# Kernel optimization log

Hardware: AMD Instinct MI355X
Metric: run time of the kernel (lower is better)

Reference implementation:

```python
import jax, jax.numpy as jnp
import numpy as np

N = 100_000      # nodes
F_IN = 256       # input features
HID = 256        # hidden dim
C = 40           # classes
E = 1_600_000    # edges
BN_EPS = 1e-5


def setup_inputs() -> dict:
    key = jax.random.key(0)
    ks = jax.random.split(key, 8)
    x = jax.random.normal(ks[0], (N, F_IN), dtype=jnp.float32)
    edge_index = jax.random.randint(ks[1], (2, E), 0, N)
    W1 = jax.random.normal(ks[2], (F_IN, HID), dtype=jnp.float32) / np.sqrt(F_IN)
    b1 = jnp.zeros((HID,), jnp.float32)
    gamma = jnp.ones((HID,), jnp.float32)
    beta = jnp.zeros((HID,), jnp.float32)
    W2 = jax.random.normal(ks[3], (HID, C), dtype=jnp.float32) / np.sqrt(HID)
    b2 = jnp.zeros((C,), jnp.float32)
    return {"x": x, "edge_index": edge_index, "W1": W1, "b1": b1,
            "gamma": gamma, "beta": beta, "W2": W2, "b2": b2}


def _gcn_propagate(h, src, dst, norm):
    # out[dst] += norm * h[src]   (symmetric-normalized aggregation, self-loops included)
    msg = norm[:, None] * h[src]                       # [E+N, D]
    return jax.ops.segment_sum(msg, dst, num_segments=N)


def reference(x, edge_index, W1, b1, gamma, beta, W2, b2):
    loops = jnp.arange(N, dtype=edge_index.dtype)
    src = jnp.concatenate([edge_index[0], loops])      # add self-loops (PyG GCNConv)
    dst = jnp.concatenate([edge_index[1], loops])
    deg = jax.ops.segment_sum(jnp.ones_like(dst, jnp.float32), dst, num_segments=N)
    dinv = jnp.where(deg > 0, jax.lax.rsqrt(deg), 0.0)
    norm = dinv[src] * dinv[dst]

    # Layer 1: GCNConv (linear without bias -> propagate -> + bias)
    h = _gcn_propagate(x @ W1, src, dst, norm) + b1    # [N, HID]
    # BatchNorm1d over nodes (training-style batch statistics, biased variance)
    mu = h.mean(axis=0)
    var = h.var(axis=0)
    h = (h - mu) * jax.lax.rsqrt(var + BN_EPS) * gamma + beta
    h = jax.nn.relu(h)                                 # dropout is identity in eval

    # Layer 2: GCNConv -> log_softmax
    out = _gcn_propagate(h @ W2, src, dst, norm) + b2  # [N, C]
    return jax.nn.log_softmax(out, axis=1)
```

## Files before the change

kernel.cpp:

```cpp
#include <hip/hip_runtime.h>
#include <math.h>

#define N_NODES 100000
#define F_IN    256
#define HID     256
#define C_OUT   40
#define N_EDGES 1600000
#define BN_EPS  1e-5f

#define CAP     64
#define NSHARD  8
#define CNT_BLOCKS  ((N_EDGES + 255) / 256)

typedef __attribute__((ext_vector_type(8))) short short8;
typedef __attribute__((ext_vector_type(8))) unsigned short ushort8v;
typedef __attribute__((ext_vector_type(4))) float f32x4;

static __device__ __forceinline__ unsigned short f2bf(float f) {
    unsigned int u = __float_as_uint(f);
    unsigned int r = u + 0x7FFFu + ((u >> 16) & 1u);
    return (unsigned short)(r >> 16);
}
static __device__ __forceinline__ float bf2f(unsigned short b) {
    return __uint_as_float(((unsigned int)b) << 16);
}

__global__ void count_castw(const int* __restrict__ dst, int* cnt8,
                            int* __restrict__ rank,
                            const float* __restrict__ W1, const float* __restrict__ W2,
                            unsigned short* __restrict__ w1t, unsigned short* __restrict__ w2t) {
    int b = blockIdx.x, t = threadIdx.x;
    if (b < CNT_BLOCKS) {
        int i = b * 256 + t;
        if (i < N_EDGES) {
            int s = b & (NSHARD - 1);
            rank[i] = atomicAdd(&cnt8[s * N_NODES + dst[i]], 1);
        }
    } else if (b < CNT_BLOCKS + 256) {
        int n = b - CNT_BLOCKS;
        w1t[(size_t)n * 256 + t] = f2bf(W1[(size_t)t * 256 + n]);
    } else {
        int n = b - CNT_BLOCKS - 256;
        w2t[(size_t)n * 256 + t] = (n < C_OUT) ? f2bf(W2[(size_t)t * C_OUT + n]) : (unsigned short)0;
    }
}

__global__ __launch_bounds__(256) void base_init(const int* __restrict__ cnt8,
                                                 int* __restrict__ base8,
                                                 int* __restrict__ cnttot,
                                                 float* __restrict__ dinv) {
    int d = blockIdx.x * 256 + threadIdx.x;
    if (d < N_NODES) {
        int run = 0;
#pragma unroll
        for (int s = 0; s < NSHARD; s++) {
            int c = cnt8[s * N_NODES + d];
            base8[s * N_NODES + d] = run;
            run += c;
        }
        cnttot[d] = run;
        dinv[d] = rsqrtf((float)(run + 1));
    }
}

__global__ __launch_bounds__(256) void scatter_sharded(const int* __restrict__ src,
                                                       const int* __restrict__ dst,
                                                       const int* __restrict__ rank,
                                                       const int* __restrict__ base8,
                                                       int* __restrict__ csr) {
    int e = blockIdx.x * 256 + threadIdx.x;
    if (e < N_EDGES) {
        int s = (e >> 8) & (NSHARD - 1);
        int d = dst[e];
        int pos = base8[s * N_NODES + d] + rank[e];
        if (pos < CAP) csr[(size_t)d * CAP + pos] = src[e];
    }
}

#define LDK 56
__global__ __launch_bounds__(256) void gemm1_mfma(const float* __restrict__ x,
                                                  const unsigned short* __restrict__ w1t,
                                                  const float* __restrict__ dinv,
                                                  unsigned short* __restrict__ hs, int M) {
    __shared__ unsigned short As[64][LDK];
    __shared__ unsigned short Bs[256][LDK];
    int tid = threadIdx.x;
    int wave = tid >> 6, lane = tid & 63;
    int m0 = blockIdx.x * 64;
    f32x4 acc[4][4] = {};

    int ar = tid >> 2, ac = (tid & 3) * 8;
    int brow = tid;
    int gr = m0 + ar;
    bool rowok = gr < M;
    const float* xrow = x + (size_t)gr * 256 + ac;
    const unsigned short* wrow = w1t + (size_t)brow * 256;

    float4 pa = make_float4(0.f,0.f,0.f,0.f), pb = pa;
    if (rowok) { pa = *(const float4*)(xrow); pb = *(const float4*)(xrow + 4); }
    ushort8v rb0 = *(const ushort8v*)(wrow);
    ushort8v rb1 = *(const ushort8v*)(wrow + 8);
    ushort8v rb2 = *(const ushort8v*)(wrow + 16);
    ushort8v rb3 = *(const ushort8v*)(wrow + 24);

    for (int k0 = 0; k0 < 256; k0 += 32) {
        {
            ushort8v u;
            u[0] = f2bf(pa.x); u[1] = f2bf(pa.y); u[2] = f2bf(pa.z); u[3] = f2bf(pa.w);
            u[4] = f2bf(pb.x); u[5] = f2bf(pb.y); u[6] = f2bf(pb.z); u[7] = f2bf(pb.w);
            if (!rowok) {
#pragma unroll
                for (int q = 0; q < 8; q++) u[q] = 0;
            }
            *(ushort8v*)&As[ar][ac] = u;
        }
        *(ushort8v*)&Bs[brow][0]  = rb0;
        *(ushort8v*)&Bs[brow][8]  = rb1;
        *(ushort8v*)&Bs[brow][16] = rb2;
        *(ushort8v*)&Bs[brow][24] = rb3;
        __syncthreads();
        if (k0 + 32 < 256) {
            if (rowok) {
                pa = *(const float4*)(xrow + k0 + 32);
                pb = *(const float4*)(xrow + k0 + 36);
            }
            const unsigned short* p = wrow + k0 + 32;
            rb0 = *(const ushort8v*)(p);
            rb1 = *(const ushort8v*)(p + 8);
            rb2 = *(const ushort8v*)(p + 16);
            rb3 = *(const ushort8v*)(p + 24);
        }
        int fr = lane & 15, fk = (lane >> 4) * 8;
        short8 a[4], b[4];
#pragma unroll
        for (int mt = 0; mt < 4; mt++) a[mt] = *(short8*)&As[mt * 16 + fr][fk];
#pragma unroll
        for (int nt = 0; nt < 4; nt++) b[nt] = *(short8*)&Bs[wave * 64 + nt * 16 + fr][fk];
#pragma unroll
        for (int mt = 0; mt < 4; mt++)
#pragma unroll
            for (int nt = 0; nt < 4; nt++)
                acc[mt][nt] = __builtin_amdgcn_mfma_f32_16x16x32_bf16(a[mt], b[nt], acc[mt][nt], 0, 0, 0);
        __syncthreads();
    }
    int fr = lane & 15, fg = lane >> 4;
#pragma unroll
    for (int mt = 0; mt < 4; mt++) {
#pragma unroll
        for (int r = 0; r < 4; r++) {
            int row = m0 + mt * 16 + fg * 4 + r;
            if (row < M) {
                float dv = dinv[row];
#pragma unroll
                for (int nt = 0; nt < 4; nt++) {
                    int col = wave * 64 + nt * 16 + fr;
                    hs[(size_t)row * 256 + col] = f2bf(acc[mt][nt][r] * dv);
                }
            }
        }
    }
}

__global__ __launch_bounds__(256) void agg256(const int* __restrict__ cnttot,
                                              const int* __restrict__ csr,
                                              const unsigned short* __restrict__ hs,
                                              const float* __restrict__ dinv,
                                              unsigned short* __restrict__ hagg) {
    int g = blockIdx.x * blockDim.x + threadIdx.x;
    int wid = g >> 6, lane = g & 63;
    if (wid >= N_NODES) return;
    int half = lane >> 5;
    int c8 = (lane & 31) * 8;
    int beg = wid * CAP;
    int end = beg + min(cnttot[wid], CAP);
    float acc[8] = {0.f, 0.f, 0.f, 0.f, 0.f, 0.f, 0.f, 0.f};
    int j = beg;
    if (j + 7 < end) {
        int sxA[4];
        ushort8v uA[4];
#pragma unroll
        for (int q = 0; q < 4; q++) sxA[q] = csr[j + 2 * q + half];
#pragma unroll
        for (int q = 0; q < 4; q++) uA[q] = *(const ushort8v*)(hs + (size_t)sxA[q] * 256 + c8);
        j += 8;
        while (j + 7 < end) {
            int sxB[4];
            ushort8v uB[4];
#pragma unroll
            for (int q = 0; q < 4; q++) sxB[q] = csr[j + 2 * q + half];
#pragma unroll
            for (int q = 0; q < 4; q++) uB[q] = *(const ushort8v*)(hs + (size_t)sxB[q] * 256 + c8);
#pragma unroll
            for (int q = 0; q < 4; q++)
#pragma unroll
                for (int e = 0; e < 8; e++) acc[e] += bf2f(uA[q][e]);
#pragma unroll
            for (int q = 0; q < 4; q++) uA[q] = uB[q];
            j += 8;
        }
#pragma unroll
        for (int q = 0; q < 4; q++)
#pragma unroll
            for (int e = 0; e < 8; e++) acc[e] += bf2f(uA[q][e]);
    }
    if (j + 3 < end) {
        int s0 = csr[j + half];
        int s1 = csr[j + 2 + half];
        ushort8v u0 = *(const ushort8v*)(hs + (size_t)s0 * 256 + c8);
        ushort8v u1 = *(const ushort8v*)(hs + (size_t)s1 * 256 + c8);
#pragma unroll
        for (int e = 0; e < 8; e++) acc[e] += bf2f(u0[e]) + bf2f(u1[e]);
        j += 4;
    }
    if (j + 1 < end) {
        int s = csr[j + half];
        ushort8v u = *(const ushort8v*)(hs + (size_t)s * 256 + c8);
#pragma unroll
        for (int e = 0; e < 8; e++) acc[e] += bf2f(u[e]);
        j += 2;
    }
    if (j < end && half == 0) {
        int s = csr[j];
        ushort8v u = *(const ushort8v*)(hs + (size_t)s * 256 + c8);
#pragma unroll
        for (int e = 0; e < 8; e++) acc[e] += bf2f(u[e]);
    }
#pragma unroll
    for (int e = 0; e < 8; e++) acc[e] += __shfl_xor(acc[e], 32);
    if (half == 0) {
        ushort8v us = *(const ushort8v*)(hs + (size_t)wid * 256 + c8);
        float dv = dinv[wid];
        ushort8v o;
#pragma unroll
        for (int e = 0; e < 8; e++) o[e] = f2bf((acc[e] + bf2f(us[e])) * dv);
        *(ushort8v*)(hagg + (size_t)wid * 256 + c8) = o;
    }
}

#define BNS_BLOCKS 1024
__global__ __launch_bounds__(256) void bn_stats_v(const unsigned short* __restrict__ h,
                                                  float* musum, float* sqsum) {
    int tid = threadIdx.x;
    int wave = tid >> 6, lane = tid & 63;
    int half = lane >> 5;
    int c8 = (lane & 31) * 8;
    int gw = blockIdx.x * 4 + wave;
    float s[8] = {0.f,0.f,0.f,0.f,0.f,0.f,0.f,0.f};
    float q2[8] = {0.f,0.f,0.f,0.f,0.f,0.f,0.f,0.f};
    for (int r = gw * 2 + half; r < N_NODES; r += BNS_BLOCKS * 4 * 2) {
        ushort8v u = *(const ushort8v*)(h + (size_t)r * 256 + c8);
#pragma unroll
        for (int e = 0; e < 8; e++) {
            float v = bf2f(u[e]);
            s[e] += v; q2[e] += v * v;
        }
    }
#pragma unroll
    for (int e = 0; e < 8; e++) {
        s[e]  += __shfl_xor(s[e], 32);
        q2[e] += __shfl_xor(q2[e], 32);
    }
    __shared__ float sS[4][256];
    __shared__ float sQ[4][256];
    if (half == 0) {
#pragma unroll
        for (int e = 0; e < 8; e++) { sS[wave][c8 + e] = s[e]; sQ[wave][c8 + e] = q2[e]; }
    }
    __syncthreads();
    float a = sS[0][tid] + sS[1][tid] + sS[2][tid] + sS[3][tid];
    float b = sQ[0][tid] + sQ[1][tid] + sQ[2][tid] + sQ[3][tid];
    atomicAdd(&musum[tid], a);
    atomicAdd(&sqsum[tid], b);
}

#define LDB2 264
__global__ __launch_bounds__(256) void gemm2_mfma(const unsigned short* __restrict__ hagg,
                                                  const unsigned short* __restrict__ w2t,
                                                  const float* __restrict__ musum,
                                                  const float* __restrict__ sqsum,
                                                  const float* __restrict__ gamma,
                                                  const float* __restrict__ beta,
                                                  const float* __restrict__ dinv,
                                                  unsigned short* __restrict__ g2b, int M) {
    __shared__ unsigned short w2s[48][LDB2];
    __shared__ unsigned short As[64][40];
    __shared__ float ss[256], sh[256];
    int tid = threadIdx.x;
    int wave = tid >> 6, lane = tid & 63;
    int m0 = blockIdx.x * 64;

    for (int i = tid; i < 48 * 32; i += 256) {
        int rrow = i >> 5, c8 = (i & 31) * 8;
        *(ushort8v*)&w2s[rrow][c8] = *(const ushort8v*)(w2t + (size_t)rrow * 256 + c8);
    }
    {
        const float invN = 1.0f / N_NODES;
        float m = musum[tid] * invN;
        float var = sqsum[tid] * invN - m * m;
        float s = gamma[tid] * rsqrtf(var + BN_EPS);
        ss[tid] = s;
        sh[tid] = beta[tid] - m * s;
    }

    f32x4 acc[3] = {};
    int arow = tid >> 2, ac0 = (tid & 3) * 8;
    int fr = lane & 15, fk = (lane >> 4) * 8;

    for (int k0 = 0; k0 < 256; k0 += 32) {
        __syncthreads();
        {
            int gr = m0 + arow;
            ushort8v u;
            if (gr < M) {
                u = *(const ushort8v*)(hagg + (size_t)gr * 256 + k0 + ac0);
#pragma unroll
                for (int q = 0; q < 8; q++) {
                    int col = k0 + ac0 + q;
                    float v = bf2f(u[q]);
                    v = fmaxf(v * ss[col] + sh[col], 0.0f);
                    u[q] = f2bf(v);
                }
            } else {
#pragma unroll
                for (int q = 0; q < 8; q++) u[q] = 0;
            }
            *(ushort8v*)&As[arow][ac0] = u;
        }
        __syncthreads();
        short8 a = *(short8*)&As[wave * 16 + fr][fk];
#pragma unroll
        for (int nt = 0; nt < 3; nt++) {
            short8 b = *(short8*)&w2s[nt * 16 + fr][k0 + fk];
            acc[nt] = __builtin_amdgcn_mfma_f32_16x16x32_bf16(a, b, acc[nt], 0, 0, 0);
        }
    }
    int fg = lane >> 4;
#pragma unroll
    for (int nt = 0; nt < 3; nt++) {
        int col = nt * 16 + fr;
        if (col < C_OUT) {
#pragma unroll
            for (int r = 0; r < 4; r++) {
                int row = m0 + wave * 16 + fg * 4 + r;
                if (row < M) g2b[(size_t)row * C_OUT + col] = f2bf(acc[nt][r] * dinv[row]);
            }
        }
    }
}

__global__ __launch_bounds__(256) void agg40_logsm(const int* __restrict__ cnttot,
                                                   const int* __restrict__ csr,
                                                   const unsigned short* __restrict__ g2b,
                                                   const float* __restrict__ dinv,
                                                   const float* __restrict__ b2,
                                                   float* __restrict__ out) {
    int gi = blockIdx.x * blockDim.x + threadIdx.x;
    int wid = gi >> 6, lane = gi & 63;
    if (wid >= N_NODES) return;
    int g = lane / 10;
    int k4 = lane - g * 10;
    bool gact = lane < 60;
    int beg = wid * CAP;
    int end = beg + min(cnttot[wid], CAP);
    float a4[4] = {0.f, 0.f, 0.f, 0.f};
    if (end > beg) {
        int jlim = end - 1;
        int j = beg;
        int s0 = csr[min(j + g, jlim)];
        ushort4 u0 = *(const ushort4*)(g2b + (size_t)s0 * C_OUT + k4 * 4);
        while (1) {
            int jn = j + 6;
            bool more = jn < end;
            int s1 = 0; ushort4 u1;
            if (more) {
                s1 = csr[min(jn + g, jlim)];
                u1 = *(const ushort4*)(g2b + (size_t)s1 * C_OUT + k4 * 4);
            }
            if (gact && j + g < end) {
                a4[0] += bf2f(u0.x); a4[1] += bf2f(u0.y);
                a4[2] += bf2f(u0.z); a4[3] += bf2f(u0.w);
            }
            if (!more) break;
            u0 = u1; j = jn;
        }
    }
#pragma unroll
    for (int e = 0; e < 4; e++) {
        float t0 = __shfl(a4[e], lane + 30);
        a4[e] += t0;
    }
#pragma unroll
    for (int e = 0; e < 4; e++) {
        float t1 = __shfl(a4[e], lane + 10);
        float t2 = __shfl(a4[e], lane + 20);
        a4[e] += t1 + t2;
    }
    bool act = lane < 10;
    float dvd = dinv[wid];
    float v[4];
    float mloc = -INFINITY;
    if (act) {
        ushort4 su = *(const ushort4*)(g2b + (size_t)wid * C_OUT + k4 * 4);
        a4[0] += bf2f(su.x); a4[1] += bf2f(su.y);
        a4[2] += bf2f(su.z); a4[3] += bf2f(su.w);
    }
#pragma unroll
    for (int e = 0; e < 4; e++) {
        v[e] = act ? a4[e] * dvd + b2[k4 * 4 + e] : -INFINITY;
        mloc = fmaxf(mloc, v[e]);
    }
#pragma unroll
    for (int o = 32; o > 0; o >>= 1) mloc = fmaxf(mloc, __shfl_xor(mloc, o));
    float sloc = 0.f;
    if (act) {
#pragma unroll
        for (int e = 0; e < 4; e++) sloc += __expf(v[e] - mloc);
    }
#pragma unroll
    for (int o = 32; o > 0; o >>= 1) sloc += __shfl_xor(sloc, o);
    float ls = __logf(sloc);
    if (act) {
        float4 o4 = make_float4(v[0] - mloc - ls, v[1] - mloc - ls,
                                v[2] - mloc - ls, v[3] - mloc - ls);
        *(float4*)(out + (size_t)wid * C_OUT + k4 * 4) = o4;
    }
}

extern "C" void kernel_launch(void* const* d_in, const int* in_sizes, int n_in,
                              void* d_out, int out_size, void* d_ws, size_t ws_size,
                              hipStream_t stream) {
    const float* x     = (const float*)d_in[0];
    const int*   ei    = (const int*)  d_in[1];
    const float* W1    = (const float*)d_in[2];
    const float* gamma = (const float*)d_in[4];
    const float* beta  = (const float*)d_in[5];
    const float* W2    = (const float*)d_in[6];
    const float* b2    = (const float*)d_in[7];
    float* out = (float*)d_out;

    const int* src = ei;
    const int* dst = ei + N_EDGES;

    unsigned short* hs    = (unsigned short*)d_ws;
    unsigned short* hagg  = hs + (size_t)N_NODES * 256;
    unsigned short* g2b   = hagg + (size_t)N_NODES * 256;
    float*          dinv  = (float*)(g2b + (size_t)N_NODES * C_OUT);
    int*            cnttot= (int*)(dinv + N_NODES);
    int*            csr   = cnttot + N_NODES;
    unsigned short* w1t   = (unsigned short*)(csr + (size_t)N_NODES * CAP);
    unsigned short* w2t   = w1t + 65536;
    float*          musum = (float*)(w2t + 48 * 256);
    float*          sqsum = musum + 256;
    int*            cnt8  = (int*)hs;
    int*            rank  = (int*)hagg;
    int*            base8 = (int*)g2b;

    hipMemsetAsync(cnt8, 0, NSHARD * N_NODES * sizeof(int), stream);
    hipMemsetAsync(musum, 0, 512 * sizeof(float), stream);

    count_castw<<<CNT_BLOCKS + 256 + 48, 256, 0, stream>>>(dst, cnt8, rank, W1, W2, w1t, w2t);
    base_init<<<(N_NODES + 255) / 256, 256, 0, stream>>>(cnt8, base8, cnttot, dinv);
    scatter_sharded<<<CNT_BLOCKS, 256, 0, stream>>>(src, dst, rank, base8, csr);

    gemm1_mfma<<<(N_NODES + 63) / 64, 256, 0, stream>>>(x, w1t, dinv, hs, N_NODES);

    int aggblk = (int)(((size_t)N_NODES * 64 + 255) / 256);
    agg256<<<aggblk, 256, 0, stream>>>(cnttot, csr, hs, dinv, hagg);

    bn_stats_v<<<BNS_BLOCKS, 256, 0, stream>>>(hagg, musum, sqsum);

    gemm2_mfma<<<(N_NODES + 63) / 64, 256, 0, stream>>>(hagg, w2t, musum, sqsum, gamma, beta, dinv, g2b, N_NODES);

    agg40_logsm<<<aggblk, 256, 0, stream>>>(cnttot, csr, g2b, dinv, b2, out);
}
```

Measured before the change: 398.8 us.

## Fuse BatchNorm statistics into aggregation epilogue and batch edge counting per thread

Removes the separate bn_stats kernel. agg256 now accumulates per-column sum and sum of squares of its bf16-rounded outputs in shared memory and atomically adds them into 8 replicated slots. gemm2 reduces those slots when it builds the BN scale and shift. The edge count and scatter kernels also process 4 edges per thread with a matching shard mapping. This saves a full re-read of the hidden activations, but adds a block barrier plus 512 float atomics per aggregation block, which could cause contention.

```diff
diff --git a/kernel.cpp b/kernel.cpp
--- a/kernel.cpp
+++ b/kernel.cpp
@@ -10,7 +10,7 @@
 
 #define CAP     64
 #define NSHARD  8
-#define CNT_BLOCKS  ((N_EDGES + 255) / 256)
+#define CNT4_BLOCKS ((N_EDGES + 1023) / 1024)
 
 typedef __attribute__((ext_vector_type(8))) short short8;
 typedef __attribute__((ext_vector_type(8))) unsigned short ushort8v;
@@ -30,17 +30,19 @@
                             const float* __restrict__ W1, const float* __restrict__ W2,
                             unsigned short* __restrict__ w1t, unsigned short* __restrict__ w2t) {
     int b = blockIdx.x, t = threadIdx.x;
-    if (b < CNT_BLOCKS) {
-        int i = b * 256 + t;
-        if (i < N_EDGES) {
-            int s = b & (NSHARD - 1);
-            rank[i] = atomicAdd(&cnt8[s * N_NODES + dst[i]], 1);
-        }
-    } else if (b < CNT_BLOCKS + 256) {
-        int n = b - CNT_BLOCKS;
+    if (b < CNT4_BLOCKS) {
+        int s = b & (NSHARD - 1);
+        int base = b * 1024 + t;
+#pragma unroll
+        for (int k = 0; k < 4; k++) {
+            int i = base + k * 256;
+            if (i < N_EDGES) rank[i] = atomicAdd(&cnt8[s * N_NODES + dst[i]], 1);
+        }
+    } else if (b < CNT4_BLOCKS + 256) {
+        int n = b - CNT4_BLOCKS;
         w1t[(size_t)n * 256 + t] = f2bf(W1[(size_t)t * 256 + n]);
     } else {
-        int n = b - CNT_BLOCKS - 256;
+        int n = b - CNT4_BLOCKS - 256;
         w2t[(size_t)n * 256 + t] = (n < C_OUT) ? f2bf(W2[(size_t)t * C_OUT + n]) : (unsigned short)0;
     }
 }
@@ -68,12 +70,16 @@
                                                        const int* __restrict__ rank,
                                                        const int* __restrict__ base8,
                                                        int* __restrict__ csr) {
-    int e = blockIdx.x * 256 + threadIdx.x;
-    if (e < N_EDGES) {
-        int s = (e >> 8) & (NSHARD - 1);
-        int d = dst[e];
-        int pos = base8[s * N_NODES + d] + rank[e];
-        if (pos < CAP) csr[(size_t)d * CAP + pos] = src[e];
+    int base = blockIdx.x * 1024 + threadIdx.x;
+#pragma unroll
+    for (int k = 0; k < 4; k++) {
+        int e = base + k * 256;
+        if (e < N_EDGES) {
+            int s = (e >> 10) & (NSHARD - 1);
+            int d = dst[e];
+            int pos = base8[s * N_NODES + d] + rank[e];
+            if (pos < CAP) csr[(size_t)d * CAP + pos] = src[e];
+        }
     }
 }
 
@@ -165,10 +171,14 @@
                                               const int* __restrict__ csr,
                                               const unsigned short* __restrict__ hs,
                                               const float* __restrict__ dinv,
-                                              unsigned short* __restrict__ hagg) {
+                                              unsigned short* __restrict__ hagg,
+                                              float* __restrict__ musum8,
+                                              float* __restrict__ sqsum8) {
+    __shared__ float sS[4][256];
+    __shared__ float sQ[4][256];
     int g = blockIdx.x * blockDim.x + threadIdx.x;
     int wid = g >> 6, lane = g & 63;
-    if (wid >= N_NODES) return;
+    int wave = threadIdx.x >> 6;
     int half = lane >> 5;
     int c8 = (lane & 31) * 8;
     int beg = wid * CAP;
@@ -231,53 +241,36 @@
         ushort8v us = *(const ushort8v*)(hs + (size_t)wid * 256 + c8);
         float dv = dinv[wid];
         ushort8v o;
-#pragma unroll
-        for (int e = 0; e < 8; e++) o[e] = f2bf((acc[e] + bf2f(us[e])) * dv);
+        float vs[8];
+#pragma unroll
+        for (int e = 0; e < 8; e++) {
+            unsigned short ob = f2bf((acc[e] + bf2f(us[e])) * dv);
+            o[e] = ob;
+            vs[e] = bf2f(ob);
+        }
         *(ushort8v*)(hagg + (size_t)wid * 256 + c8) = o;
-    }
-}
-
-#define BNS_BLOCKS 1024
-__global__ __launch_bounds__(256) void bn_stats_v(const unsigned short* __restrict__ h,
-                                                  float* musum, float* sqsum) {
-    int tid = threadIdx.x;
-    int wave = tid >> 6, lane = tid & 63;
-    int half = lane >> 5;
-    int c8 = (lane & 31) * 8;
-    int gw = blockIdx.x * 4 + wave;
-    float s[8] = {0.f,0.f,0.f,0.f,0.f,0.f,0.f,0.f};
-    float q2[8] = {0.f,0.f,0.f,0.f,0.f,0.f,0.f,0.f};
-    for (int r = gw * 2 + half; r < N_NODES; r += BNS_BLOCKS * 4 * 2) {
-        ushort8v u = *(const ushort8v*)(h + (size_t)r * 256 + c8);
 #pragma unroll
         for (int e = 0; e < 8; e++) {
-            float v = bf2f(u[e]);
-            s[e] += v; q2[e] += v * v;
-        }
-    }
-#pragma unroll
-    for (int e = 0; e < 8; e++) {
-        s[e]  += __shfl_xor(s[e], 32);
-        q2[e] += __shfl_xor(q2[e], 32);
-    }
-    __shared__ float sS[4][256];
-    __shared__ float sQ[4][256];
-    if (half == 0) {
-#pragma unroll
-        for (int e = 0; e < 8; e++) { sS[wave][c8 + e] = s[e]; sQ[wave][c8 + e] = q2[e]; }
+            sS[wave][c8 + e] = vs[e];
+            sQ[wave][c8 + e] = vs[e] * vs[e];
+        }
     }
     __syncthreads();
-    float a = sS[0][tid] + sS[1][tid] + sS[2][tid] + sS[3][tid];
-    float b = sQ[0][tid] + sQ[1][tid] + sQ[2][tid] + sQ[3][tid];
-    atomicAdd(&musum[tid], a);
-    atomicAdd(&sqsum[tid], b);
+    {
+        int tid = threadIdx.x;
+        float a = sS[0][tid] + sS[1][tid] + sS[2][tid] + sS[3][tid];
+        float b = sQ[0][tid] + sQ[1][tid] + sQ[2][tid] + sQ[3][tid];
+        int rep = (blockIdx.x & 7) * 256 + tid;
+        atomicAdd(&musum8[rep], a);
+        atomicAdd(&sqsum8[rep], b);
+    }
 }
 
 #define LDB2 264
 __global__ __launch_bounds__(256) void gemm2_mfma(const unsigned short* __restrict__ hagg,
                                                   const unsigned short* __restrict__ w2t,
-                                                  const float* __restrict__ musum,
-                                                  const float* __restrict__ sqsum,
+                                                  const float* __restrict__ musum8,
+                                                  const float* __restrict__ sqsum8,
                                                   const float* __restrict__ gamma,
                                                   const float* __restrict__ beta,
                                                   const float* __restrict__ dinv,
@@ -294,9 +287,15 @@
         *(ushort8v*)&w2s[rrow][c8] = *(const ushort8v*)(w2t + (size_t)rrow * 256 + c8);
     }
     {
+        float msum = 0.f, qsum = 0.f;
+#pragma unroll
+        for (int r = 0; r < 8; r++) {
+            msum += musum8[r * 256 + tid];
+            qsum += sqsum8[r * 256 + tid];
+        }
         const float invN = 1.0f / N_NODES;
-        float m = musum[tid] * invN;
-        float var = sqsum[tid] * invN - m * m;
+        float m = msum * invN;
+        float var = qsum * invN - m * m;
         float s = gamma[tid] * rsqrtf(var + BN_EPS);
         ss[tid] = s;
         sh[tid] = beta[tid] - m * s;
@@ -449,27 +448,25 @@
     int*            csr   = cnttot + N_NODES;
     unsigned short* w1t   = (unsigned short*)(csr + (size_t)N_NODES * CAP);
     unsigned short* w2t   = w1t + 65536;
-    float*          musum = (float*)(w2t + 48 * 256);
-    float*          sqsum = musum + 256;
+    float*          musum8= (float*)(w2t + 48 * 256);
+    float*          sqsum8= musum8 + 8 * 256;
     int*            cnt8  = (int*)hs;
     int*            rank  = (int*)hagg;
     int*            base8 = (int*)g2b;
 
     hipMemsetAsync(cnt8, 0, NSHARD * N_NODES * sizeof(int), stream);
-    hipMemsetAsync(musum, 0, 512 * sizeof(float), stream);
-
-    count_castw<<<CNT_BLOCKS + 256 + 48, 256, 0, stream>>>(dst, cnt8, rank, W1, W2, w1t, w2t);
+    hipMemsetAsync(musum8, 0, 2 * 8 * 256 * sizeof(float), stream);
+
+    count_castw<<<CNT4_BLOCKS + 256 + 48, 256, 0, stream>>>(dst, cnt8, rank, W1, W2, w1t, w2t);
     base_init<<<(N_NODES + 255) / 256, 256, 0, stream>>>(cnt8, base8, cnttot, dinv);
-    scatter_sharded<<<CNT_BLOCKS, 256, 0, stream>>>(src, dst, rank, base8, csr);
+    scatter_sharded<<<CNT4_BLOCKS, 256, 0, stream>>>(src, dst, rank, base8, csr);
 
     gemm1_mfma<<<(N_NODES + 63) / 64, 256, 0, stream>>>(x, w1t, dinv, hs, N_NODES);
 
     int aggblk = (int)(((size_t)N_NODES * 64 + 255) / 256);
-    agg256<<<aggblk, 256, 0, stream>>>(cnttot, csr, hs, dinv, hagg);
-
-    bn_stats_v<<<BNS_BLOCKS, 256, 0, stream>>>(hagg, musum, sqsum);
-
-    gemm2_mfma<<<(N_NODES + 63) / 64, 256, 0, stream>>>(hagg, w2t, musum, sqsum, gamma, beta, dinv, g2b, N_NODES);
+    agg256<<<aggblk, 256, 0, stream>>>(cnttot, csr, hs, dinv, hagg, musum8, sqsum8);
+
+    gemm2_mfma<<<(N_NODES + 63) / 64, 256, 0, stream>>>(hagg, w2t, musum8, sqsum8, gamma, beta, dinv, g2b, N_NODES);
 
     agg40_logsm<<<aggblk, 256, 0, stream>>>(cnttot, csr, g2b, dinv, b2, out);
 }
```

Result: no change. 399.9 us (+0.3%).
